# Performance work log

Hardware: AMD Instinct MI355X
Metric: run time of the kernel (lower is better)

## Reference

```python
import jax, jax.numpy as jnp
import numpy as np


def setup_inputs() -> dict:
    key = jax.random.key(0)
    k1, k2 = jax.random.split(key)
    bilateral_grid = jax.random.normal(k1, (8, 12, 8, 16, 16), dtype=jnp.float32)  # [N,C,D,Hg,Wg]
    guidemap = jax.random.uniform(k2, (8, 1, 1024, 1024), dtype=jnp.float32)       # [N,1,H,W] in [0,1]
    return {"bilateral_grid": bilateral_grid, "guidemap": guidemap}


def _bilateral_slice(grid, guide):
    # grid: [N, gh, gw, gd, C]; guide: [N, h, w] in [0,1]
    N, gh, gw, gd, C = grid.shape
    h, w = guide.shape[1], guide.shape[2]
    dt = grid.dtype
    # continuous grid coords (HDRNet convention: pixel centers, scale = grid/img)
    gx = (jnp.arange(w, dtype=dt) + 0.5) * (gw / w)   # [w]
    gy = (jnp.arange(h, dtype=dt) + 0.5) * (gh / h)   # [h]
    gz = guide * gd                                    # [N,h,w]
    fx = jnp.floor(gx - 0.5); fy = jnp.floor(gy - 0.5); fz = jnp.floor(gz - 0.5)
    wx1 = gx - 0.5 - fx; wy1 = gy - 0.5 - fy; wz1 = gz - 0.5 - fz  # tent weights
    x0 = jnp.clip(fx, 0, gw - 1).astype(jnp.int32); x1 = jnp.clip(fx + 1, 0, gw - 1).astype(jnp.int32)
    y0 = jnp.clip(fy, 0, gh - 1).astype(jnp.int32); y1 = jnp.clip(fy + 1, 0, gh - 1).astype(jnp.int32)
    z0 = jnp.clip(fz, 0, gd - 1).astype(jnp.int32); z1 = jnp.clip(fz + 1, 0, gd - 1).astype(jnp.int32)
    n_idx = jnp.arange(N)[:, None, None]

    def corner(yi, xi, zi):
        # gather -> [N, h, w, C]
        return grid[n_idx, yi[None, :, None], xi[None, None, :], zi]

    out = jnp.zeros((N, h, w, C), dtype=dt)
    for zi, wz in ((z0, 1.0 - wz1), (z1, wz1)):            # wz: [N,h,w]
        for yi, wy in ((y0, 1.0 - wy1), (y1, wy1)):        # wy: [h]
            for xi, wx in ((x0, 1.0 - wx1), (x1, wx1)):    # wx: [w]
                wgt = (wy[None, :, None] * wx[None, None, :] * wz)[..., None]
                out = out + wgt * corner(yi, xi, zi)
    return out  # [N,h,w,C]


def reference(bilateral_grid, guidemap):
    grid = jnp.transpose(bilateral_grid, (0, 3, 4, 2, 1))  # [N,Hg,Wg,D,C]
    guide = guidemap[:, 0]                                  # [N,H,W]
    coeffs = _bilateral_slice(grid, guide)                  # [N,H,W,C]
    return jnp.transpose(coeffs, (0, 3, 1, 2))              # [N,C,H,W]
```

## Files before the change

### kernel.cpp

```cpp
#include <hip/hip_runtime.h>
#include <hip/hip_bf16.h>


#define N_ 8
#define C_ 12
#define GD 8
#define GH 16
#define GW 16
#define H_ 1024
#define W_ 1024

__global__ void transpose_grid_kernel(const float* __restrict__ in,
                                      float* __restrict__ out) {
    int idx = blockIdx.x * 256 + threadIdx.x;
    int c = idx % C_;
    int r = idx / C_;
    int z = r & (GD - 1); r >>= 3;
    int x = r & (GW - 1); r >>= 4;
    int y = r & (GH - 1);
    int n = r >> 4;
    size_t src = ((((size_t)n * C_ + c) * GD + z) * GH + y) * GW + x;
    out[idx] = in[src];
}

template <bool USE_T>
__global__ __launch_bounds__(256) void slice_kernel(
        const float* __restrict__ grid_raw,
        const float* __restrict__ grid_t,
        const float* __restrict__ guide,
        float* __restrict__ out)
{
    const int x = blockIdx.x * 256 + threadIdx.x;
    const int y = blockIdx.y;
    const int n = blockIdx.z;

    const float gv = guide[((size_t)n * H_ + y) * W_ + x];

    const float gx = ((float)x + 0.5f) * (1.0f / 64.0f);
    const float gy = ((float)y + 0.5f) * (1.0f / 64.0f);
    const float gz = gv * (float)GD;

    const float fx = floorf(gx - 0.5f);
    const float fy = floorf(gy - 0.5f);
    const float fz = floorf(gz - 0.5f);

    const float wx1 = gx - 0.5f - fx;
    const float wy1 = gy - 0.5f - fy;
    const float wz1 = gz - 0.5f - fz;

    const int x0 = (int)fminf(fmaxf(fx,        0.0f), (float)(GW - 1));
    const int x1 = (int)fminf(fmaxf(fx + 1.0f, 0.0f), (float)(GW - 1));
    const int y0 = (int)fminf(fmaxf(fy,        0.0f), (float)(GH - 1));
    const int y1 = (int)fminf(fmaxf(fy + 1.0f, 0.0f), (float)(GH - 1));
    const int z0 = (int)fminf(fmaxf(fz,        0.0f), (float)(GD - 1));
    const int z1 = (int)fminf(fmaxf(fz + 1.0f, 0.0f), (float)(GD - 1));

    const int   zs[2]  = { z0, z1 };
    const float wzs[2] = { 1.0f - wz1, wz1 };
    const int   ys[2]  = { y0, y1 };
    const float wys[2] = { 1.0f - wy1, wy1 };
    const int   xs[2]  = { x0, x1 };
    const float wxs[2] = { 1.0f - wx1, wx1 };

    float acc[C_];
#pragma unroll
    for (int c = 0; c < C_; ++c) acc[c] = 0.0f;

#pragma unroll
    for (int zz = 0; zz < 2; ++zz) {
#pragma unroll
        for (int yy = 0; yy < 2; ++yy) {
#pragma unroll
            for (int xx = 0; xx < 2; ++xx) {
                const float wgt = wys[yy] * wxs[xx] * wzs[zz];
                if (USE_T) {
                    const float4* p = (const float4*)grid_t +
                        ((((size_t)n * GH + ys[yy]) * GW + xs[xx]) * GD + zs[zz]) * 3;
                    const float4 a = p[0];
                    const float4 b = p[1];
                    const float4 d = p[2];
                    acc[0]  += wgt * a.x;  acc[1]  += wgt * a.y;
                    acc[2]  += wgt * a.z;  acc[3]  += wgt * a.w;
                    acc[4]  += wgt * b.x;  acc[5]  += wgt * b.y;
                    acc[6]  += wgt * b.z;  acc[7]  += wgt * b.w;
                    acc[8]  += wgt * d.x;  acc[9]  += wgt * d.y;
                    acc[10] += wgt * d.z;  acc[11] += wgt * d.w;
                } else {
                    const float* p = grid_raw +
                        (((size_t)n * C_) * GD + zs[zz]) * (GH * GW) +
                        ys[yy] * GW + xs[xx];
#pragma unroll
                    for (int c = 0; c < C_; ++c)
                        acc[c] += wgt * p[(size_t)c * (GD * GH * GW)];
                }
            }
        }
    }

    const size_t ob = ((size_t)n * C_) * (size_t)(H_ * W_) + (size_t)y * W_ + x;
#pragma unroll
    for (int c = 0; c < C_; ++c)
        out[ob + (size_t)c * (H_ * W_)] = acc[c];
}

extern "C" void kernel_launch(void* const* d_in, const int* in_sizes, int n_in,
                              void* d_out, int out_size, void* d_ws, size_t ws_size,
                              hipStream_t stream) {
    const float* grid_raw = (const float*)d_in[0];
    const float* guide    = (const float*)d_in[1];
    float* out = (float*)d_out;

    const size_t t_bytes = (size_t)N_ * GH * GW * GD * C_ * sizeof(float);

    const dim3 sgrid(W_ / 256, H_, N_);
    const dim3 sblock(256);

    if (ws_size >= t_bytes) {
        float* grid_t = (float*)d_ws;
        transpose_grid_kernel<<<dim3((N_ * GH * GW * GD * C_) / 256), dim3(256),
                                0, stream>>>(grid_raw, grid_t);
        slice_kernel<true><<<sgrid, sblock, 0, stream>>>(grid_raw, grid_t, guide, out);
    } else {
        slice_kernel<false><<<sgrid, sblock, 0, stream>>>(grid_raw, nullptr, guide, out);
    }
}
```

Before: 529.6 us.

## Stage per-row grid slab in LDS and process four pixels per thread

Removes the separate grid transpose kernel. Each block now handles one full image row: it loads the two needed grid rows (y0,y1) for all x, z and c into shared memory in channel-last layout, then each thread computes four consecutive pixels and writes them with vectorized nontemporal stores. The aim is to replace scattered global gathers with LDS reads, cut the extra kernel launch, and make output writes wider. In exchange it adds a sync and an uncoalesced strided global load per block, and the scattered LDS reads can hit bank conflicts.

```diff
diff --git a/kernel.cpp b/kernel.cpp
--- a/kernel.cpp
+++ b/kernel.cpp
@@ -10,97 +10,102 @@
 #define H_ 1024
 #define W_ 1024
 
-__global__ void transpose_grid_kernel(const float* __restrict__ in,
-                                      float* __restrict__ out) {
-    int idx = blockIdx.x * 256 + threadIdx.x;
-    int c = idx % C_;
-    int r = idx / C_;
-    int z = r & (GD - 1); r >>= 3;
-    int x = r & (GW - 1); r >>= 4;
-    int y = r & (GH - 1);
-    int n = r >> 4;
-    size_t src = ((((size_t)n * C_ + c) * GD + z) * GH + y) * GW + x;
-    out[idx] = in[src];
-}
+typedef float v4f __attribute__((ext_vector_type(4)));
 
-template <bool USE_T>
-__global__ __launch_bounds__(256) void slice_kernel(
+__global__ __launch_bounds__(256) void slice_row_kernel(
         const float* __restrict__ grid_raw,
-        const float* __restrict__ grid_t,
         const float* __restrict__ guide,
         float* __restrict__ out)
 {
-    const int x = blockIdx.x * 256 + threadIdx.x;
-    const int y = blockIdx.y;
-    const int n = blockIdx.z;
+    __shared__ float slab[2 * GW * GD * C_];
 
-    const float gv = guide[((size_t)n * H_ + y) * W_ + x];
+    const int tid = threadIdx.x;
+    const int y   = blockIdx.y;
+    const int n   = blockIdx.z;
 
-    const float gx = ((float)x + 0.5f) * (1.0f / 64.0f);
-    const float gy = ((float)y + 0.5f) * (1.0f / 64.0f);
-    const float gz = gv * (float)GD;
-
-    const float fx = floorf(gx - 0.5f);
-    const float fy = floorf(gy - 0.5f);
-    const float fz = floorf(gz - 0.5f);
-
-    const float wx1 = gx - 0.5f - fx;
+    const float gy  = ((float)y + 0.5f) * (1.0f / 64.0f);
+    const float fy  = floorf(gy - 0.5f);
     const float wy1 = gy - 0.5f - fy;
-    const float wz1 = gz - 0.5f - fz;
-
-    const int x0 = (int)fminf(fmaxf(fx,        0.0f), (float)(GW - 1));
-    const int x1 = (int)fminf(fmaxf(fx + 1.0f, 0.0f), (float)(GW - 1));
     const int y0 = (int)fminf(fmaxf(fy,        0.0f), (float)(GH - 1));
     const int y1 = (int)fminf(fmaxf(fy + 1.0f, 0.0f), (float)(GH - 1));
-    const int z0 = (int)fminf(fmaxf(fz,        0.0f), (float)(GD - 1));
-    const int z1 = (int)fminf(fmaxf(fz + 1.0f, 0.0f), (float)(GD - 1));
-
-    const int   zs[2]  = { z0, z1 };
-    const float wzs[2] = { 1.0f - wz1, wz1 };
-    const int   ys[2]  = { y0, y1 };
-    const float wys[2] = { 1.0f - wy1, wy1 };
-    const int   xs[2]  = { x0, x1 };
-    const float wxs[2] = { 1.0f - wx1, wx1 };
-
-    float acc[C_];
-#pragma unroll
-    for (int c = 0; c < C_; ++c) acc[c] = 0.0f;
 
 #pragma unroll
-    for (int zz = 0; zz < 2; ++zz) {
+    for (int k = 0; k < 12; ++k) {
+        int eid = k * 256 + tid;
+        int x   = eid & (GW - 1);
+        int r   = eid >> 4;
+        int yy  = r & 1;  r >>= 1;
+        int z   = r & (GD - 1);
+        int c   = r >> 3;
+        int ysel = yy ? y1 : y0;
+        slab[((yy * GW + x) * GD + z) * C_ + c] =
+            grid_raw[(((size_t)n * C_ + c) * GD + z) * (GH * GW) + ysel * GW + x];
+    }
+    __syncthreads();
+
+    const float wys[2] = { 1.0f - wy1, wy1 };
+
+    const v4f g4 = ((const v4f*)(guide + ((size_t)n * H_ + y) * W_))[tid];
+
+    float vout[C_][4];
+
 #pragma unroll
-        for (int yy = 0; yy < 2; ++yy) {
+    for (int j = 0; j < 4; ++j) {
+        const int px = tid * 4 + j;
+
+        const float gx  = ((float)px + 0.5f) * (1.0f / 64.0f);
+        const float fx  = floorf(gx - 0.5f);
+        const float wx1 = gx - 0.5f - fx;
+        const int x0 = (int)fminf(fmaxf(fx,        0.0f), (float)(GW - 1));
+        const int x1 = (int)fminf(fmaxf(fx + 1.0f, 0.0f), (float)(GW - 1));
+
+        const float gz  = g4[j] * (float)GD;
+        const float fz  = floorf(gz - 0.5f);
+        const float wz1 = gz - 0.5f - fz;
+        const int z0 = (int)fminf(fmaxf(fz,        0.0f), (float)(GD - 1));
+        const int z1 = (int)fminf(fmaxf(fz + 1.0f, 0.0f), (float)(GD - 1));
+
+        const int   zs[2]  = { z0, z1 };
+        const float wzs[2] = { 1.0f - wz1, wz1 };
+        const int   xs[2]  = { x0, x1 };
+        const float wxs[2] = { 1.0f - wx1, wx1 };
+
+        float acc[C_];
 #pragma unroll
-            for (int xx = 0; xx < 2; ++xx) {
-                const float wgt = wys[yy] * wxs[xx] * wzs[zz];
-                if (USE_T) {
-                    const float4* p = (const float4*)grid_t +
-                        ((((size_t)n * GH + ys[yy]) * GW + xs[xx]) * GD + zs[zz]) * 3;
-                    const float4 a = p[0];
-                    const float4 b = p[1];
-                    const float4 d = p[2];
+        for (int c = 0; c < C_; ++c) acc[c] = 0.0f;
+
+#pragma unroll
+        for (int zz = 0; zz < 2; ++zz) {
+#pragma unroll
+            for (int yy = 0; yy < 2; ++yy) {
+#pragma unroll
+                for (int xx = 0; xx < 2; ++xx) {
+                    const float wgt = wys[yy] * wxs[xx] * wzs[zz];
+                    const v4f* s4 = (const v4f*)
+                        &slab[((yy * GW + xs[xx]) * GD + zs[zz]) * C_];
+                    const v4f a = s4[0];
+                    const v4f b = s4[1];
+                    const v4f d = s4[2];
                     acc[0]  += wgt * a.x;  acc[1]  += wgt * a.y;
                     acc[2]  += wgt * a.z;  acc[3]  += wgt * a.w;
                     acc[4]  += wgt * b.x;  acc[5]  += wgt * b.y;
                     acc[6]  += wgt * b.z;  acc[7]  += wgt * b.w;
                     acc[8]  += wgt * d.x;  acc[9]  += wgt * d.y;
                     acc[10] += wgt * d.z;  acc[11] += wgt * d.w;
-                } else {
-                    const float* p = grid_raw +
-                        (((size_t)n * C_) * GD + zs[zz]) * (GH * GW) +
-                        ys[yy] * GW + xs[xx];
-#pragma unroll
-                    for (int c = 0; c < C_; ++c)
-                        acc[c] += wgt * p[(size_t)c * (GD * GH * GW)];
                 }
             }
         }
+
+#pragma unroll
+        for (int c = 0; c < C_; ++c) vout[c][j] = acc[c];
     }
 
-    const size_t ob = ((size_t)n * C_) * (size_t)(H_ * W_) + (size_t)y * W_ + x;
+    const size_t ob = ((size_t)n * C_) * (size_t)(H_ * W_) + (size_t)y * W_ + (size_t)tid * 4;
 #pragma unroll
-    for (int c = 0; c < C_; ++c)
-        out[ob + (size_t)c * (H_ * W_)] = acc[c];
+    for (int c = 0; c < C_; ++c) {
+        v4f v = { vout[c][0], vout[c][1], vout[c][2], vout[c][3] };
+        __builtin_nontemporal_store(v, (v4f*)(out + ob + (size_t)c * (H_ * W_)));
+    }
 }
 
 extern "C" void kernel_launch(void* const* d_in, const int* in_sizes, int n_in,
@@ -110,17 +115,7 @@
     const float* guide    = (const float*)d_in[1];
     float* out = (float*)d_out;
 
-    const size_t t_bytes = (size_t)N_ * GH * GW * GD * C_ * sizeof(float);
-
-    const dim3 sgrid(W_ / 256, H_, N_);
-    const dim3 sblock(256);
-
-    if (ws_size >= t_bytes) {
-        float* grid_t = (float*)d_ws;
-        transpose_grid_kernel<<<dim3((N_ * GH * GW * GD * C_) / 256), dim3(256),
-                                0, stream>>>(grid_raw, grid_t);
-        slice_kernel<true><<<sgrid, sblock, 0, stream>>>(grid_raw, grid_t, guide, out);
-    } else {
-        slice_kernel<false><<<sgrid, sblock, 0, stream>>>(grid_raw, nullptr, guide, out);
-    }
+    const dim3 grid(1, H_, N_);
+    const dim3 block(256);
+    slice_row_kernel<<<grid, block, 0, stream>>>(grid_raw, guide, out);
 }
```

Result: faster. 459.8 us (-13.2%).
